# Performance work log

Hardware: AMD Instinct MI355X
Metric: run time of the kernel (lower is better)

Reference implementation:

```python
import jax, jax.numpy as jnp
import numpy as np
import itertools

# ---- static configuration (matches init_kwargs) ----
LS = [0, 1, 2, 3]            # spherical harmonic degrees, parity (-1)^l
MUL = 128                    # channel multiplicity of hklm / output
N_EDGES = 16384
DIMS = [2 * l + 1 for l in LS]
Y_DIM = sum(DIMS)                        # 16
H_DIM = sum(d * MUL for d in DIMS)       # 2048
Y_OFF = np.cumsum([0] + DIMS).tolist()
H_OFF = np.cumsum([0] + [d * MUL for d in DIMS]).tolist()

# ---- real-basis O(3) Clebsch-Gordan coefficients (numpy, setup-time) ----
def _su2_generators(l):
    m = np.arange(-l, l + 1)
    Lz = np.diag(m).astype(np.complex128)
    vals = np.sqrt(l * (l + 1) - m[:-1] * (m[:-1] + 1))
    Lp = np.zeros((2 * l + 1, 2 * l + 1), np.complex128)
    Lp[np.arange(1, 2 * l + 1), np.arange(2 * l)] = vals
    Lm = Lp.T.copy()
    return (Lp + Lm) / 2.0, (Lp - Lm) / 2.0j, Lz

def _c2r(l):
    # unitary change of basis: complex SH -> real SH
    d = 2 * l + 1
    U = np.zeros((d, d), np.complex128)
    U[l, l] = 1.0
    s2 = 1.0 / np.sqrt(2.0)
    for m in range(1, l + 1):
        U[l + m, l + m] = (-1) ** m * s2
        U[l + m, l - m] = s2
        U[l - m, l + m] = -1j * (-1) ** m * s2
        U[l - m, l - m] = 1j * s2
    return U

def _real_generators(l):
    U = _c2r(l)
    return [np.real(-1j * (U @ L @ U.conj().T)) for L in _su2_generators(l)]

def _cg(l1, l2, l3):
    # invariant tensor = null space of the summed infinitesimal rotation action
    G1, G2, G3 = _real_generators(l1), _real_generators(l2), _real_generators(l3)
    d1, d2, d3 = 2 * l1 + 1, 2 * l2 + 1, 2 * l3 + 1
    I1, I2, I3 = np.eye(d1), np.eye(d2), np.eye(d3)
    rows = []
    for k in range(3):
        rows.append(np.kron(np.kron(G1[k], I2), I3)
                    + np.kron(np.kron(I1, G2[k]), I3)
                    + np.kron(np.kron(I1, I2), G3[k]))
    K = np.concatenate(rows, axis=0)
    _, s, Vt = np.linalg.svd(K)
    c = Vt[-1].reshape(d1, d2, d3)
    c = c / np.linalg.norm(c)
    c = c * np.sign(c.reshape(-1)[np.argmax(np.abs(c))])  # deterministic sign
    return c

PATHS = []
_CG_LIST = []
for (i1, l1), (i2, l2), (i3, l3) in itertools.product(enumerate(LS), enumerate(LS), enumerate(LS)):
    # triangle inequality + O3 parity selection rule ((-1)^l parities)
    if abs(l1 - l2) <= l3 <= l1 + l2 and (l1 + l2 + l3) % 2 == 0:
        PATHS.append((i1, i2, i3))
        _CG_LIST.append(_cg(l1, l2, l3))
N_PATHS = len(PATHS)                    # 23
W_DIM = N_PATHS * MUL                   # 2944
CG_OFF = np.cumsum([0] + [c.size for c in _CG_LIST]).tolist()
CGC_NP = np.concatenate([c.reshape(-1) for c in _CG_LIST]).astype(np.float32)


def setup_inputs() -> dict:
    key = jax.random.key(0)
    k1, k2, k3 = jax.random.split(key, 3)
    return {
        "Ylm": jax.random.normal(k1, (N_EDGES, Y_DIM), jnp.float32),
        "hklm": jax.random.normal(k2, (N_EDGES, H_DIM), jnp.float32),
        "weight": jax.random.normal(k3, (N_EDGES, W_DIM), jnp.float32),
        "CGC": jnp.asarray(CGC_NP),   # registered buffer in the torch module
    }


def reference(Ylm, hklm, weight, CGC):
    # segmented tensor product 'abcu,a,bu,cu' with per-path weight fused in:
    # out[n, c, u] += sum_{a,b} CG_p[a,b,c] * w_p[n,u] * Y[n,a] * h[n,b,u]
    N = Ylm.shape[0]
    out = jnp.zeros((N, H_DIM), Ylm.dtype)
    for p, (i1, i2, i3) in enumerate(PATHS):
        d1, d2, d3 = DIMS[i1], DIMS[i2], DIMS[i3]
        cg = CGC[CG_OFF[p]:CG_OFF[p + 1]].reshape(d1, d2, d3)
        y = Ylm[:, Y_OFF[i1]:Y_OFF[i1] + d1]
        h = hklm[:, H_OFF[i2]:H_OFF[i2] + d2 * MUL].reshape(N, d2, MUL)
        w = weight[:, p * MUL:(p + 1) * MUL]
        z = jnp.einsum('abc,na,nbu->ncu', cg, y, h) * w[:, None, :]
        out = out.at[:, H_OFF[i3]:H_OFF[i3] + d3 * MUL].add(z.reshape(N, d3 * MUL))
    return out
```

## Files before the change

### kernel.cpp

```cpp
#include <hip/hip_runtime.h>


#define BS 256
#define EPB 2
#define TPE 128
#define YD 16
#define HD 2048
#define WD 2944
#define NP 23
#define NROW 99

typedef float f4 __attribute__((ext_vector_type(4)));

#define FOR_PATHS(X) \
  X(0, 0,0,0,    0,  0) \
  X(1, 0,1,1,    1,  1) \
  X(2, 0,2,2,   10,  4) \
  X(3, 0,3,3,   35,  9) \
  X(4, 1,0,1,   84, 16) \
  X(5, 1,1,0,   93, 19) \
  X(6, 1,1,2,  102, 20) \
  X(7, 1,2,1,  147, 25) \
  X(8, 1,2,3,  192, 28) \
  X(9, 1,3,2,  297, 35) \
  X(10,2,0,2,  402, 40) \
  X(11,2,1,1,  427, 45) \
  X(12,2,1,3,  472, 48) \
  X(13,2,2,0,  577, 55) \
  X(14,2,2,2,  602, 56) \
  X(15,2,3,1,  727, 61) \
  X(16,2,3,3,  832, 64) \
  X(17,3,0,3, 1077, 71) \
  X(18,3,1,2, 1126, 78) \
  X(19,3,2,1, 1231, 83) \
  X(20,3,2,3, 1336, 86) \
  X(21,3,3,0, 1581, 93) \
  X(22,3,3,2, 1630, 94)

__host__ __device__ constexpr int coff(int l) {
  return l == 0 ? 0 : (l == 1 ? 1 : (l == 2 ? 4 : 9));
}

__global__ __launch_bounds__(BS, 6) void etp_kernel(
    const float* __restrict__ Y, const float* __restrict__ H,
    const float* __restrict__ W, const float* __restrict__ CG,
    float* __restrict__ O) {
  const int g = threadIdx.x >> 7;
  const int u = threadIdx.x & 127;
  const size_t n = (size_t)blockIdx.x * EPB + g;

  __shared__ __align__(16) float Bsm[EPB][NROW * 8];
  __shared__ float ysm[EPB][YD];

  { const int t = threadIdx.x;
    if (t < EPB * YD) {
      const int e = t >> 4, c = t & 15;
      ysm[e][c] = Y[(size_t)(blockIdx.x * EPB + e) * YD + c];
    } }
  __syncthreads();

#define BUILD(P, L1, L2, L3, CGO, RO) { \
    constexpr int d1 = 2*(L1)+1, d2 = 2*(L2)+1, d3 = 2*(L3)+1; \
    if (u < d2 * d3) { \
      const int m3 = u / d2, m2 = u - m3 * d2; \
      float s = 0.f; \
      _Pragma("unroll") \
      for (int a = 0; a < d1; ++a) \
        s += CG[(CGO) + (a * d2 + m2) * d3 + m3] * ysm[g][coff(L1) + a]; \
      Bsm[g][((RO) + m3) * 8 + m2] = s; \
    } }
  FOR_PATHS(BUILD)
#undef BUILD
  __syncthreads();

  const float* __restrict__ Hn = H + n * HD + u;
  const float* __restrict__ Wn = W + n * WD + u;
  float* __restrict__ On = O + n * HD + u;

  float h[YD];
#pragma unroll
  for (int c = 0; c < YD; ++c) h[c] = Hn[c * TPE];
  float w[NP];
#pragma unroll
  for (int p = 0; p < NP; ++p) w[p] = Wn[p * TPE];
#pragma unroll
  for (int c = 0; c < YD; ++c) asm volatile("" : "+v"(h[c]));
#pragma unroll
  for (int p = 0; p < NP; ++p) asm volatile("" : "+v"(w[p]));

  float acc[YD];
#pragma unroll
  for (int c = 0; c < YD; ++c) acc[c] = 0.f;

#define DOP(P, L1, L2, L3, CGO, RO) { \
    constexpr int d2 = 2*(L2)+1, d3 = 2*(L3)+1; \
    const float wv = w[P]; \
    _Pragma("unroll") \
    for (int m3 = 0; m3 < d3; ++m3) { \
      const f4* row = (const f4*)&Bsm[g][((RO) + m3) * 8]; \
      float br[8]; \
      *(f4*)&br[0] = row[0]; \
      if (d2 > 4) *(f4*)&br[4] = row[1]; \
      float s = 0.f; \
      _Pragma("unroll") \
      for (int m2 = 0; m2 < d2; ++m2) s += br[m2] * h[coff(L2) + m2]; \
      acc[coff(L3) + m3] += s * wv; \
    } }
  FOR_PATHS(DOP)
#undef DOP

#pragma unroll
  for (int c = 0; c < YD; ++c)
    __builtin_nontemporal_store(acc[c], &On[c * TPE]);
}

extern "C" void kernel_launch(void* const* d_in, const int* in_sizes, int n_in,
                              void* d_out, int out_size, void* d_ws, size_t ws_size,
                              hipStream_t stream) {
  const float* Y  = (const float*)d_in[0];
  const float* H  = (const float*)d_in[1];
  const float* W  = (const float*)d_in[2];
  const float* CG = (const float*)d_in[3];
  float* O = (float*)d_out;

  const int n_edges = in_sizes[0] / YD;
  etp_kernel<<<n_edges / EPB, BS, 0, stream>>>(Y, H, W, CG, O);
}
```

Baseline: 95.36 us.

## Broadcast per-edge CG-Y products via readlane instead of shared-memory rows

Each wavefront now builds the per-path CG·Y matrices in lane registers from a shared-memory copy of the CG table, then broadcasts entries with readlane into the contraction instead of writing and re-reading a shared B matrix. The second block barrier goes away. H and W loads are grouped by input degree so fewer values stay live at once, and launch bounds rise from 6 to 7 waves. The cost is many scalar readlane instructions and a per-block copy of the whole CG table into LDS.

```diff
diff --git a/kernel.cpp b/kernel.cpp
--- a/kernel.cpp
+++ b/kernel.cpp
@@ -7,107 +7,132 @@
 #define YD 16
 #define HD 2048
 #define WD 2944
-#define NP 23
-#define NROW 99
-
-typedef float f4 __attribute__((ext_vector_type(4)));
-
-#define FOR_PATHS(X) \
-  X(0, 0,0,0,    0,  0) \
-  X(1, 0,1,1,    1,  1) \
-  X(2, 0,2,2,   10,  4) \
-  X(3, 0,3,3,   35,  9) \
-  X(4, 1,0,1,   84, 16) \
-  X(5, 1,1,0,   93, 19) \
-  X(6, 1,1,2,  102, 20) \
-  X(7, 1,2,1,  147, 25) \
-  X(8, 1,2,3,  192, 28) \
-  X(9, 1,3,2,  297, 35) \
-  X(10,2,0,2,  402, 40) \
-  X(11,2,1,1,  427, 45) \
-  X(12,2,1,3,  472, 48) \
-  X(13,2,2,0,  577, 55) \
-  X(14,2,2,2,  602, 56) \
-  X(15,2,3,1,  727, 61) \
-  X(16,2,3,3,  832, 64) \
-  X(17,3,0,3, 1077, 71) \
-  X(18,3,1,2, 1126, 78) \
-  X(19,3,2,1, 1231, 83) \
-  X(20,3,2,3, 1336, 86) \
-  X(21,3,3,0, 1581, 93) \
-  X(22,3,3,2, 1630, 94)
+#define CGTOT 1875
 
 __host__ __device__ constexpr int coff(int l) {
   return l == 0 ? 0 : (l == 1 ? 1 : (l == 2 ? 4 : 9));
 }
 
-__global__ __launch_bounds__(BS, 6) void etp_kernel(
-    const float* __restrict__ Y, const float* __restrict__ H,
-    const float* __restrict__ W, const float* __restrict__ CG,
-    float* __restrict__ O) {
+__device__ __forceinline__ float rl(float v, int lane) {
+  return __int_as_float(__builtin_amdgcn_readlane(__float_as_int(v), lane));
+}
+
+__global__ __launch_bounds__(BS, 7) void etp_kernel(
+    const float* __restrict__ Yg, const float* __restrict__ Hg,
+    const float* __restrict__ Wg, const float* __restrict__ CGg,
+    float* __restrict__ Og) {
+  __shared__ float cgs[CGTOT];
+  for (int i = threadIdx.x; i < CGTOT; i += BS) cgs[i] = CGg[i];
+
   const int g = threadIdx.x >> 7;
   const int u = threadIdx.x & 127;
+  const int l = threadIdx.x & 63;
   const size_t n = (size_t)blockIdx.x * EPB + g;
 
-  __shared__ __align__(16) float Bsm[EPB][NROW * 8];
-  __shared__ float ysm[EPB][YD];
-
-  { const int t = threadIdx.x;
-    if (t < EPB * YD) {
-      const int e = t >> 4, c = t & 15;
-      ysm[e][c] = Y[(size_t)(blockIdx.x * EPB + e) * YD + c];
-    } }
   __syncthreads();
 
-#define BUILD(P, L1, L2, L3, CGO, RO) { \
-    constexpr int d1 = 2*(L1)+1, d2 = 2*(L2)+1, d3 = 2*(L3)+1; \
-    if (u < d2 * d3) { \
-      const int m3 = u / d2, m2 = u - m3 * d2; \
-      float s = 0.f; \
-      _Pragma("unroll") \
-      for (int a = 0; a < d1; ++a) \
-        s += CG[(CGO) + (a * d2 + m2) * d3 + m3] * ysm[g][coff(L1) + a]; \
-      Bsm[g][((RO) + m3) * 8 + m2] = s; \
-    } }
-  FOR_PATHS(BUILD)
-#undef BUILD
-  __syncthreads();
+  float yv = Yg[n * YD + (l & 15)];
+  float yy[YD];
+#pragma unroll
+  for (int c = 0; c < YD; ++c) yy[c] = rl(yv, c);
 
-  const float* __restrict__ Hn = H + n * HD + u;
-  const float* __restrict__ Wn = W + n * WD + u;
-  float* __restrict__ On = O + n * HD + u;
-
-  float h[YD];
-#pragma unroll
-  for (int c = 0; c < YD; ++c) h[c] = Hn[c * TPE];
-  float w[NP];
-#pragma unroll
-  for (int p = 0; p < NP; ++p) w[p] = Wn[p * TPE];
-#pragma unroll
-  for (int c = 0; c < YD; ++c) asm volatile("" : "+v"(h[c]));
-#pragma unroll
-  for (int p = 0; p < NP; ++p) asm volatile("" : "+v"(w[p]));
+  const float* __restrict__ Hn = Hg + n * HD + u;
+  const float* __restrict__ Wn = Wg + n * WD + u;
+  float* __restrict__ On = Og + n * HD + u;
 
   float acc[YD];
 #pragma unroll
   for (int c = 0; c < YD; ++c) acc[c] = 0.f;
 
-#define DOP(P, L1, L2, L3, CGO, RO) { \
-    constexpr int d2 = 2*(L2)+1, d3 = 2*(L3)+1; \
-    const float wv = w[P]; \
+#define BLD(vB, L1, D2, D3, CGO) \
+  if (l < (D2) * (D3)) { \
+    float s_ = 0.f; \
     _Pragma("unroll") \
-    for (int m3 = 0; m3 < d3; ++m3) { \
-      const f4* row = (const f4*)&Bsm[g][((RO) + m3) * 8]; \
-      float br[8]; \
-      *(f4*)&br[0] = row[0]; \
-      if (d2 > 4) *(f4*)&br[4] = row[1]; \
-      float s = 0.f; \
+    for (int a = 0; a < 2 * (L1) + 1; ++a) \
+      s_ += cgs[(CGO) + (a * (D2) + m2g) * (D3) + m3g] * yy[coff(L1) + a]; \
+    vB = s_; \
+  }
+
+#define CONS(vB, D2, D3, L3, WV) { \
+    _Pragma("unroll") \
+    for (int m3 = 0; m3 < (D3); ++m3) { \
+      float s_ = 0.f; \
       _Pragma("unroll") \
-      for (int m2 = 0; m2 < d2; ++m2) s += br[m2] * h[coff(L2) + m2]; \
-      acc[coff(L3) + m3] += s * wv; \
+      for (int m2 = 0; m2 < (D2); ++m2) \
+        s_ += rl(vB, m3 * (D2) + m2) * hh[m2]; \
+      acc[coff(L3) + m3] += s_ * (WV); \
     } }
-  FOR_PATHS(DOP)
-#undef DOP
+
+  {
+    float hh[1], wg[4];
+    hh[0] = Hn[0 * TPE];
+    wg[0] = Wn[0 * TPE];  wg[1] = Wn[4 * TPE];
+    wg[2] = Wn[10 * TPE]; wg[3] = Wn[17 * TPE];
+    asm volatile("" : "+v"(hh[0]), "+v"(wg[0]), "+v"(wg[1]), "+v"(wg[2]),
+                      "+v"(wg[3]));
+    const int m3g = l, m2g = 0;
+    float b0 = 0.f, b4 = 0.f, b10 = 0.f, b17 = 0.f;
+    BLD(b0, 0, 1, 1, 0)      BLD(b4, 1, 1, 3, 84)
+    BLD(b10, 2, 1, 5, 402)   BLD(b17, 3, 1, 7, 1077)
+    CONS(b0, 1, 1, 0, wg[0])   CONS(b4, 1, 3, 1, wg[1])
+    CONS(b10, 1, 5, 2, wg[2])  CONS(b17, 1, 7, 3, wg[3])
+  }
+  {
+    float hh[3], wg[6];
+#pragma unroll
+    for (int m = 0; m < 3; ++m) hh[m] = Hn[(1 + m) * TPE];
+    wg[0] = Wn[1 * TPE];  wg[1] = Wn[5 * TPE];  wg[2] = Wn[6 * TPE];
+    wg[3] = Wn[11 * TPE]; wg[4] = Wn[12 * TPE]; wg[5] = Wn[18 * TPE];
+    asm volatile("" : "+v"(hh[0]), "+v"(hh[1]), "+v"(hh[2]),
+                      "+v"(wg[0]), "+v"(wg[1]), "+v"(wg[2]),
+                      "+v"(wg[3]), "+v"(wg[4]), "+v"(wg[5]));
+    const int m3g = l / 3, m2g = l - m3g * 3;
+    float b1 = 0.f, b5 = 0.f, b6 = 0.f, b11 = 0.f, b12 = 0.f, b18 = 0.f;
+    BLD(b1, 0, 3, 3, 1)      BLD(b5, 1, 3, 1, 93)    BLD(b6, 1, 3, 5, 102)
+    BLD(b11, 2, 3, 3, 427)   BLD(b12, 2, 3, 7, 472)  BLD(b18, 3, 3, 5, 1126)
+    CONS(b1, 3, 3, 1, wg[0])   CONS(b5, 3, 1, 0, wg[1])   CONS(b6, 3, 5, 2, wg[2])
+    CONS(b11, 3, 3, 1, wg[3])  CONS(b12, 3, 7, 3, wg[4])  CONS(b18, 3, 5, 2, wg[5])
+  }
+  {
+    float hh[5], wg[7];
+#pragma unroll
+    for (int m = 0; m < 5; ++m) hh[m] = Hn[(4 + m) * TPE];
+    wg[0] = Wn[2 * TPE];  wg[1] = Wn[7 * TPE];  wg[2] = Wn[8 * TPE];
+    wg[3] = Wn[13 * TPE]; wg[4] = Wn[14 * TPE]; wg[5] = Wn[19 * TPE];
+    wg[6] = Wn[20 * TPE];
+    asm volatile("" : "+v"(hh[0]), "+v"(hh[1]), "+v"(hh[2]), "+v"(hh[3]),
+                      "+v"(hh[4]),
+                      "+v"(wg[0]), "+v"(wg[1]), "+v"(wg[2]), "+v"(wg[3]),
+                      "+v"(wg[4]), "+v"(wg[5]), "+v"(wg[6]));
+    const int m3g = l / 5, m2g = l - m3g * 5;
+    float b2 = 0.f, b7 = 0.f, b8 = 0.f, b13 = 0.f, b14 = 0.f, b19 = 0.f,
+          b20 = 0.f;
+    BLD(b2, 0, 5, 5, 10)     BLD(b7, 1, 5, 3, 147)   BLD(b8, 1, 5, 7, 192)
+    BLD(b13, 2, 5, 1, 577)   BLD(b14, 2, 5, 5, 602)  BLD(b19, 3, 5, 3, 1231)
+    BLD(b20, 3, 5, 7, 1336)
+    CONS(b2, 5, 5, 2, wg[0])   CONS(b7, 5, 3, 1, wg[1])   CONS(b8, 5, 7, 3, wg[2])
+    CONS(b13, 5, 1, 0, wg[3])  CONS(b14, 5, 5, 2, wg[4])  CONS(b19, 5, 3, 1, wg[5])
+    CONS(b20, 5, 7, 3, wg[6])
+  }
+  {
+    float hh[7], wg[6];
+#pragma unroll
+    for (int m = 0; m < 7; ++m) hh[m] = Hn[(9 + m) * TPE];
+    wg[0] = Wn[3 * TPE];  wg[1] = Wn[9 * TPE];  wg[2] = Wn[15 * TPE];
+    wg[3] = Wn[16 * TPE]; wg[4] = Wn[21 * TPE]; wg[5] = Wn[22 * TPE];
+    asm volatile("" : "+v"(hh[0]), "+v"(hh[1]), "+v"(hh[2]), "+v"(hh[3]),
+                      "+v"(hh[4]), "+v"(hh[5]), "+v"(hh[6]),
+                      "+v"(wg[0]), "+v"(wg[1]), "+v"(wg[2]), "+v"(wg[3]),
+                      "+v"(wg[4]), "+v"(wg[5]));
+    const int m3g = l / 7, m2g = l - m3g * 7;
+    float b3 = 0.f, b9 = 0.f, b15 = 0.f, b16 = 0.f, b21 = 0.f, b22 = 0.f;
+    BLD(b3, 0, 7, 7, 35)     BLD(b9, 1, 7, 5, 297)   BLD(b15, 2, 7, 3, 727)
+    BLD(b16, 2, 7, 7, 832)   BLD(b21, 3, 7, 1, 1581) BLD(b22, 3, 7, 5, 1630)
+    CONS(b3, 7, 7, 3, wg[0])   CONS(b9, 7, 5, 2, wg[1])   CONS(b15, 7, 3, 1, wg[2])
+    CONS(b16, 7, 7, 3, wg[3])  CONS(b21, 7, 1, 0, wg[4])  CONS(b22, 7, 5, 2, wg[5])
+  }
+#undef BLD
+#undef CONS
 
 #pragma unroll
   for (int c = 0; c < YD; ++c)
```

After: 101.6 us. +6.5%, slower.
